# Kernel tuning notes

Hardware: AMD Instinct MI355X
Metric: run time of the kernel (lower is better)

The kernel has to match this reference:

```python
import jax, jax.numpy as jnp
import numpy as np

ALPHA = 3.0   # self.alpha
TAU = 0.1     # contrastive temperature
K = 8         # configs.k (top-k hyperedges per node)


def _scale(x, w, ehy, enod):
    """One scale of incidence_matrix_learn.
    x: [B, L, D] series tokens; w: [ws, D] word tokens;
    ehy: [H, D] hyperedge embedding table; enod: [N, D] node embedding table, N = L + ws.
    Returns (binary incidence matrix [N, H] float32, scalar contrastive loss).
    """
    B = x.shape[0]
    # concat_all[i]: cat(x.permute(0,2,1), word_expanded) -> [B, D, N]
    we = jnp.broadcast_to(w.T[None], (B,) + w.T.shape)          # [B, D, ws]
    concat = jnp.concatenate([jnp.transpose(x, (0, 2, 1)), we], axis=-1)  # [B, D, N]
    N, H = enod.shape[0], ehy.shape[0]
    # adjacency: softmax(relu(alpha * nodeec @ hyperen.T)) along hyperedge dim
    a = enod @ ehy.T                                            # [N, H]
    adj = jax.nn.softmax(jax.nn.relu(ALPHA * a), axis=-1)
    # top-k mask + threshold > 0.5 -> binary incidence matrix
    k = min(H, K)
    _, idx = jax.lax.top_k(adj, k)                              # [N, k]
    mask = jnp.zeros_like(adj).at[jnp.arange(N)[:, None], idx].set(1.0)
    adj_bin = ((adj * mask) > 0.5).astype(jnp.float32)          # [N, H]
    # positives: nodes sharing any hyperedge (build_pos_indices_from_edge_index),
    # equivalent to (A A^T > 0) with self excluded; dropping all-zero columns is a no-op here
    P = (adj_bin @ adj_bin.T > 0) & ~jnp.eye(N, dtype=bool)     # [N, N]
    cnt = P.sum(axis=1)                                         # positives per node
    # acl_loss_batched, vectorized over batch and nodes
    nodes = jnp.transpose(concat, (0, 2, 1))                    # [B, N, D]
    nrm = nodes / jnp.maximum(jnp.linalg.norm(nodes, axis=-1, keepdims=True), 1e-12)
    sim = jnp.einsum('bnd,bmd->bnm', nrm, nrm) / TAU            # [B, N, N]
    denom = jax.nn.logsumexp(sim, axis=-1)                      # [B, N]
    pos_mean = jnp.einsum('bnm,nm->bn', sim, P.astype(sim.dtype)) / jnp.maximum(cnt, 1)
    valid = cnt > 0                                             # [N]
    loss_sum = jnp.sum(jnp.where(valid[None, :], denom - pos_mean, 0.0))
    vc = B * valid.sum()
    loss = jnp.where(vc > 0, loss_sum / jnp.maximum(vc, 1), 0.0)
    return adj_bin, loss


def setup_inputs() -> dict:
    key = jax.random.key(0)
    ks = jax.random.split(key, 8)
    B, D = 64, 512
    return dict(
        x0=jax.random.normal(ks[0], (B, 512, D), dtype=jnp.float32),
        x1=jax.random.normal(ks[1], (B, 256, D), dtype=jnp.float32),
        word0=jax.random.normal(ks[2], (128, D), dtype=jnp.float32),
        word1=jax.random.normal(ks[3], (128, D), dtype=jnp.float32),
        embhy0=jax.random.normal(ks[4], (128, D), dtype=jnp.float32),
        embhy1=jax.random.normal(ks[5], (64, D), dtype=jnp.float32),
        embnod0=jax.random.normal(ks[6], (640, D), dtype=jnp.float32),
        embnod1=jax.random.normal(ks[7], (384, D), dtype=jnp.float32),
    )


def reference(x0, x1, word0, word1, embhy0, embhy1, embnod0, embnod1):
    a0, l0 = _scale(x0, word0, embhy0, embnod0)
    a1, l1 = _scale(x1, word1, embhy1, embnod1)
    return (a0, a1, l0 + l1)
```

## Files before the change

### kernel.cpp

```cpp
#include <hip/hip_runtime.h>


#define DDIM 512
#define BATCH 64
#define NGID 65536

typedef __attribute__((ext_vector_type(8))) short short8;
typedef __attribute__((ext_vector_type(4))) float f32x4;

__constant__ int PAIR_SCALE[21] = {0,0,0,0,0,0,0,0,0,0,0,0,0,0,0, 1,1,1,1,1,1};
__constant__ int PAIR_TU[21]    = {0,0,0,0,0,1,1,1,1,2,2,2,3,3,4, 0,0,0,1,1,2};
__constant__ int PAIR_TV[21]    = {0,1,2,3,4,1,2,3,4,2,3,4,3,4,4, 0,1,2,1,2,2};

__device__ __forceinline__ unsigned short f2bf(float f) {
  unsigned int u = __float_as_uint(f);
  u += 0x7fffu + ((u >> 16) & 1u);
  return (unsigned short)(u >> 16);
}

__device__ __forceinline__ void async16(const void* g, void* l) {
  __builtin_amdgcn_global_load_lds(
      (const __attribute__((address_space(1))) unsigned int*)g,
      (__attribute__((address_space(3))) unsigned int*)l, 16, 0, 0);
}

__global__ __launch_bounds__(256) void prep_kernel(
    const float* __restrict__ enod0, const float* __restrict__ ehy0,
    const float* __restrict__ enod1, const float* __restrict__ ehy1,
    float* __restrict__ adj0, float* __restrict__ adj1,
    int* __restrict__ labels0, int* __restrict__ labels1,
    const float* __restrict__ x0, const float* __restrict__ w0,
    const float* __restrict__ x1, const float* __restrict__ w1,
    unsigned short* __restrict__ nhat0, unsigned short* __restrict__ nhat1,
    float* __restrict__ acc, int* __restrict__ ticket) {
  const int t = threadIdx.x;
  if (blockIdx.x < 1024) {
    if (blockIdx.x == 0 && t == 0) { acc[0] = 0.f; acc[1] = 0.f; ticket[0] = 0; }
    const bool s0 = blockIdx.x < 640;
    const int n = s0 ? blockIdx.x : blockIdx.x - 640;
    const int H = s0 ? 128 : 64;
    const float* enod = s0 ? enod0 : enod1;
    const float* ehy = s0 ? ehy0 : ehy1;
    float* out_adj = s0 ? adj0 : adj1;
    int* labels = s0 ? labels0 : labels1;
    __shared__ float erow[DDIM];
    __shared__ float red[128];
    __shared__ int lab;
    if (t < 128) ((float4*)erow)[t] = ((const float4*)(enod + (size_t)n * DDIM))[t];
    if (t == 0) lab = -1;
    __syncthreads();
    float v = 0.f;
    if (t < H) {
      const float4* hr = (const float4*)(ehy + (size_t)t * DDIM);
      float a = 0.f;
      #pragma unroll 8
      for (int d = 0; d < DDIM / 4; ++d) {
        float4 h = hr[d];
        float4 e = ((const float4*)erow)[d];
        a = fmaf(h.x, e.x, a); a = fmaf(h.y, e.y, a);
        a = fmaf(h.z, e.z, a); a = fmaf(h.w, e.w, a);
      }
      v = fmaxf(0.f, 3.0f * a);
    }
    if (t < 128) red[t] = v;
    __syncthreads();
    for (int s = 64; s > 0; s >>= 1) {
      if (t < s) red[t] = fmaxf(red[t], red[t + s]);
      __syncthreads();
    }
    const float mx = red[0];
    __syncthreads();
    const float e = (t < H) ? __expf(v - mx) : 0.f;
    if (t < 128) red[t] = e;
    __syncthreads();
    for (int s = 64; s > 0; s >>= 1) {
      if (t < s) red[t] += red[t + s];
      __syncthreads();
    }
    const float sum = red[0];
    if (t < H) {
      const float adj = e / sum;
      const float bin = (adj > 0.5f) ? 1.0f : 0.0f;
      out_adj[(size_t)n * H + t] = bin;
      if (bin > 0.f) lab = t;
    }
    __syncthreads();
    if (t == 0) labels[n] = lab;
  } else {
    const int wave = t >> 6;
    const int lane = t & 63;
    const int g = (blockIdx.x - 1024) * 4 + wave;
    const bool s0 = g < BATCH * 640;
    const int gg = s0 ? g : g - BATCH * 640;
    const int N = s0 ? 640 : 384;
    const int L = s0 ? 512 : 256;
    const float* x = s0 ? x0 : x1;
    const float* w = s0 ? w0 : w1;
    unsigned short* nhat = s0 ? nhat0 : nhat1;
    const int b = gg / N;
    const int n = gg - b * N;
    const float* src = (n < L) ? (x + ((size_t)b * L + n) * DDIM)
                               : (w + (size_t)(n - L) * DDIM);
    const float4* rowp = (const float4*)src;
    const float4 v0 = rowp[lane];
    const float4 v1 = rowp[lane + 64];
    float ss = v0.x * v0.x + v0.y * v0.y + v0.z * v0.z + v0.w * v0.w +
               v1.x * v1.x + v1.y * v1.y + v1.z * v1.z + v1.w * v1.w;
    #pragma unroll
    for (int off = 32; off > 0; off >>= 1) ss += __shfl_xor(ss, off);
    const float rinv = 1.0f / fmaxf(sqrtf(ss), 1e-12f);
    ushort4 o0, o1;
    o0.x = f2bf(v0.x * rinv); o0.y = f2bf(v0.y * rinv);
    o0.z = f2bf(v0.z * rinv); o0.w = f2bf(v0.w * rinv);
    o1.x = f2bf(v1.x * rinv); o1.y = f2bf(v1.y * rinv);
    o1.z = f2bf(v1.z * rinv); o1.w = f2bf(v1.w * rinv);
    ushort4* op = (ushort4*)(nhat + ((size_t)b * N + n) * DDIM);
    op[lane] = o0;
    op[lane + 64] = o1;
  }
}

__global__ __launch_bounds__(256) void lse_kernel(
    const unsigned short* __restrict__ nhat0, const int* __restrict__ labels0,
    const unsigned short* __restrict__ nhat1, const int* __restrict__ labels1,
    float2* __restrict__ sp) {
  __shared__ short8 Abuf[3][512];
  __shared__ short8 Bbuf[3][512];
  __shared__ int labU[128], labV[128];
  __shared__ float2 rowBuf[128][2];
  __shared__ float2 colBuf[128][2];

  const int tid = threadIdx.x;
  const int p = blockIdx.x >> 6;
  const int b = blockIdx.x & 63;
  const bool s0 = PAIR_SCALE[p] == 0;
  const int tu = PAIR_TU[p], tv = PAIR_TV[p];
  const bool diag = (tu == tv);
  const int N = s0 ? 640 : 384;
  const unsigned short* nhat = s0 ? nhat0 : nhat1;
  const int* labels = s0 ? labels0 : labels1;
  const int gbase = s0 ? b * 640 : 40960 + b * 384;
  const size_t base = (size_t)b * N * DDIM;

  const int w = tid >> 6, lane = tid & 63;
  const int wr = w >> 1, wc = w & 1;
  const int lrow = lane & 15, lq = lane >> 4;

  if (tid < 128) labU[tid] = labels[tu * 128 + tid];
  else labV[tid - 128] = labels[tv * 128 + (tid - 128)];

  const unsigned short* Asrc = nhat + base + (size_t)tu * 128 * DDIM;
  const unsigned short* Bsrc = nhat + base + (size_t)tv * 128 * DDIM;

  #define STAGE(slot, cc)                                                    \
    do {                                                                     \
      _Pragma("unroll")                                                      \
      for (int i = 0; i < 2; ++i) {                                          \
        const int f = w * 2 + i;                                             \
        const size_t so = (size_t)(f * 16 + lrow) * DDIM + (cc) * 32 + lq * 8;\
        async16(Asrc + so, &Abuf[slot][f * 64]);                             \
        async16(Bsrc + so, &Bbuf[slot][f * 64]);                             \
      }                                                                      \
    } while (0)

  f32x4 acc[4][4];
  #pragma unroll
  for (int mi = 0; mi < 4; ++mi)
    #pragma unroll
    for (int ni = 0; ni < 4; ++ni) acc[mi][ni] = (f32x4){0.f, 0.f, 0.f, 0.f};

  STAGE(0, 0);
  STAGE(1, 1);

  #pragma unroll
  for (int c = 0; c < 16; ++c) {
    if (c < 15) asm volatile("s_waitcnt vmcnt(4)" ::: "memory");
    else        asm volatile("s_waitcnt vmcnt(0)" ::: "memory");
    __builtin_amdgcn_s_barrier();
    if (c < 14) STAGE((c + 2) % 3, c + 2);
    const short8* Ab = &Abuf[c % 3][0];
    const short8* Bb = &Bbuf[c % 3][0];
    short8 am[4], bn[4];
    #pragma unroll
    for (int mi = 0; mi < 4; ++mi) am[mi] = Ab[(wr * 4 + mi) * 64 + lane];
    #pragma unroll
    for (int ni = 0; ni < 4; ++ni) bn[ni] = Bb[(wc * 4 + ni) * 64 + lane];
    #pragma unroll
    for (int mi = 0; mi < 4; ++mi)
      #pragma unroll
      for (int ni = 0; ni < 4; ++ni)
        acc[mi][ni] = __builtin_amdgcn_mfma_f32_16x16x32_bf16(
            am[mi], bn[ni], acc[mi][ni], 0, 0, 0);
  }
  #undef STAGE

  float rSE[4][4], rPOS[4][4];
  float cSE[4] = {0.f, 0.f, 0.f, 0.f};
  float cPOS[4] = {0.f, 0.f, 0.f, 0.f};
  int labn[4][4], labm[4];
  #pragma unroll
  for (int mi = 0; mi < 4; ++mi)
    #pragma unroll
    for (int r = 0; r < 4; ++r) {
      rSE[mi][r] = 0.f; rPOS[mi][r] = 0.f;
      labn[mi][r] = labU[wr * 64 + mi * 16 + lq * 4 + r];
    }
  #pragma unroll
  for (int ni = 0; ni < 4; ++ni) labm[ni] = labV[wc * 64 + ni * 16 + lrow];

  #pragma unroll
  for (int mi = 0; mi < 4; ++mi) {
    const int u_loc = wr * 64 + mi * 16 + lq * 4;
    #pragma unroll
    for (int ni = 0; ni < 4; ++ni) {
      const int v_loc = wc * 64 + ni * 16 + lrow;
      #pragma unroll
      for (int r = 0; r < 4; ++r) {
        const float sim = acc[mi][ni][r] * 10.0f;
        const float e = __expf(sim - 10.0f);
        rSE[mi][r] += e;
        const bool match = (labn[mi][r] >= 0) && (labm[ni] == labn[mi][r]);
        const bool self = diag && (u_loc + r == v_loc);
        if (match && !self) rPOS[mi][r] += sim;
        if (!diag) {
          cSE[ni] += e;
          if (match) cPOS[ni] += sim;
        }
      }
    }
  }

  #pragma unroll
  for (int off = 1; off <= 8; off <<= 1)
    #pragma unroll
    for (int mi = 0; mi < 4; ++mi)
      #pragma unroll
      for (int r = 0; r < 4; ++r) {
        rSE[mi][r] += __shfl_xor(rSE[mi][r], off);
        rPOS[mi][r] += __shfl_xor(rPOS[mi][r], off);
      }
  if (lrow == 0) {
    #pragma unroll
    for (int mi = 0; mi < 4; ++mi)
      #pragma unroll
      for (int r = 0; r < 4; ++r) {
        float2 st; st.x = rSE[mi][r]; st.y = rPOS[mi][r];
        rowBuf[wr * 64 + mi * 16 + lq * 4 + r][wc] = st;
      }
  }
  if (!diag) {
    #pragma unroll
    for (int off = 16; off <= 32; off <<= 1)
      #pragma unroll
      for (int ni = 0; ni < 4; ++ni) {
        cSE[ni] += __shfl_xor(cSE[ni], off);
        cPOS[ni] += __shfl_xor(cPOS[ni], off);
      }
    if (lane < 16) {
      #pragma unroll
      for (int ni = 0; ni < 4; ++ni) {
        float2 st; st.x = cSE[ni]; st.y = cPOS[ni];
        colBuf[wc * 64 + ni * 16 + lrow][wr] = st;
      }
    }
  }
  __syncthreads();
  if (tid < 128) {
    const float2 ra = rowBuf[tid][0], rb = rowBuf[tid][1];
    float2 st; st.x = ra.x + rb.x; st.y = ra.y + rb.y;
    sp[(size_t)tv * NGID + gbase + tu * 128 + tid] = st;
    if (!diag) {
      const float2 ca = colBuf[tid][0], cb = colBuf[tid][1];
      float2 ct; ct.x = ca.x + cb.x; ct.y = ca.y + cb.y;
      sp[(size_t)tu * NGID + gbase + tv * 128 + tid] = ct;
    }
  }
}

__global__ __launch_bounds__(256) void loss_reduce(
    const float2* __restrict__ sp, const int* __restrict__ labels0,
    const int* __restrict__ labels1, float* __restrict__ acc,
    int* __restrict__ ticket, float* __restrict__ lossp) {
  __shared__ int lab0[640], lab1[384];
  __shared__ int hist0[128], hist1[64];
  __shared__ int vcS[2];
  __shared__ float r0[4], r1[4];
  const int t = threadIdx.x;
  if (t < 128) hist0[t] = 0;
  else if (t < 192) hist1[t - 128] = 0;
  if (t < 2) vcS[t] = 0;
  for (int i = t; i < 640; i += 256) lab0[i] = labels0[i];
  for (int i = t; i < 384; i += 256) lab1[i] = labels1[i];
  __syncthreads();
  for (int i = t; i < 640; i += 256)
    if (lab0[i] >= 0) atomicAdd(&hist0[lab0[i]], 1);
  for (int i = t; i < 384; i += 256)
    if (lab1[i] >= 0) atomicAdd(&hist1[lab1[i]], 1);
  __syncthreads();
  int lv0 = 0, lv1 = 0;
  for (int i = t; i < 640; i += 256)
    if (lab0[i] >= 0 && hist0[lab0[i]] >= 2) ++lv0;
  for (int i = t; i < 384; i += 256)
    if (lab1[i] >= 0 && hist1[lab1[i]] >= 2) ++lv1;
  if (lv0 > 0) atomicAdd(&vcS[0], lv0);
  if (lv1 > 0) atomicAdd(&vcS[1], lv1);
  __syncthreads();

  float l0 = 0.f, l1 = 0.f;
  for (int g = blockIdx.x * 256 + t; g < NGID; g += 64 * 256) {
    const bool is0 = g < 40960;
    const int n = is0 ? (g % 640) : ((g - 40960) % 384);
    const int nslots = is0 ? 5 : 3;
    float se = 0.f, pos = 0.f;
    for (int s = 0; s < nslots; ++s) {
      const float2 v = sp[(size_t)s * NGID + g];
      se += v.x; pos += v.y;
    }
    const int lb = is0 ? lab0[n] : lab1[n];
    const int c = (lb >= 0) ? ((is0 ? hist0[lb] : hist1[lb]) - 1) : 0;
    if (c > 0) {
      const float v = (10.0f + logf(se)) - pos / (float)c;
      if (is0) l0 += v; else l1 += v;
    }
  }
  #pragma unroll
  for (int off = 32; off > 0; off >>= 1) {
    l0 += __shfl_xor(l0, off);
    l1 += __shfl_xor(l1, off);
  }
  if ((t & 63) == 0) { r0[t >> 6] = l0; r1[t >> 6] = l1; }
  __syncthreads();
  if (t == 0) {
    atomicAdd(&acc[0], r0[0] + r0[1] + r0[2] + r0[3]);
    atomicAdd(&acc[1], r1[0] + r1[1] + r1[2] + r1[3]);
    __threadfence();
    const int done = atomicAdd(ticket, 1);
    if (done == 63) {
      const float a0v = atomicAdd(&acc[0], 0.0f);
      const float a1v = atomicAdd(&acc[1], 0.0f);
      float l = 0.f;
      if (vcS[0] > 0) l += a0v / (float)(BATCH * vcS[0]);
      if (vcS[1] > 0) l += a1v / (float)(BATCH * vcS[1]);
      lossp[0] = l;
    }
  }
}

extern "C" void kernel_launch(void* const* d_in, const int* in_sizes, int n_in,
                              void* d_out, int out_size, void* d_ws,
                              size_t ws_size, hipStream_t stream) {
  const float* x0 = (const float*)d_in[0];
  const float* x1 = (const float*)d_in[1];
  const float* w0 = (const float*)d_in[2];
  const float* w1 = (const float*)d_in[3];
  const float* ehy0 = (const float*)d_in[4];
  const float* ehy1 = (const float*)d_in[5];
  const float* enod0 = (const float*)d_in[6];
  const float* enod1 = (const float*)d_in[7];

  float* out = (float*)d_out;
  float* adj0 = out;
  float* adj1 = out + 640 * 128;
  float* lossp = out + 640 * 128 + 384 * 64;

  unsigned short* nhat0 = (unsigned short*)d_ws;
  unsigned short* nhat1 = nhat0 + (size_t)BATCH * 640 * DDIM;
  int* ip = (int*)(nhat1 + (size_t)BATCH * 384 * DDIM);
  int* labels0 = ip;
  int* labels1 = labels0 + 640;
  int* ticket = labels1 + 384;
  float* acc = (float*)(ticket + 1);
  float2* sp = (float2*)((((size_t)(acc + 2)) + 255) & ~(size_t)255);

  prep_kernel<<<1024 + 16384, 256, 0, stream>>>(
      enod0, ehy0, enod1, ehy1, adj0, adj1, labels0, labels1,
      x0, w0, x1, w1, nhat0, nhat1, acc, ticket);
  lse_kernel<<<1344, 256, 0, stream>>>(nhat0, labels0, nhat1, labels1, sp);
  loss_reduce<<<64, 256, 0, stream>>>(sp, labels0, labels1, acc, ticket,
                                      lossp);
}
```

Measured before the change: 237.7 us.

## Grid-stride normalize rows and overlay LDS buffers in lse kernel

The normalization part of prep_kernel now runs 1024 blocks, each looping over 16 rows per wave, instead of launching 16384 blocks. This cuts block launch overhead. In lse_kernel, the separate shared arrays become one 48KB buffer that the reduction buffers reuse after a barrier, and labels are loaded straight from global memory into registers. The smaller LDS footprint could allow more resident blocks, but each thread now holds extra registers, and the grid-stride loop does not overlap row loads across iterations.

```diff
diff --git a/kernel.cpp b/kernel.cpp
--- a/kernel.cpp
+++ b/kernel.cpp
@@ -89,34 +89,42 @@
   } else {
     const int wave = t >> 6;
     const int lane = t & 63;
-    const int g = (blockIdx.x - 1024) * 4 + wave;
-    const bool s0 = g < BATCH * 640;
-    const int gg = s0 ? g : g - BATCH * 640;
-    const int N = s0 ? 640 : 384;
-    const int L = s0 ? 512 : 256;
-    const float* x = s0 ? x0 : x1;
-    const float* w = s0 ? w0 : w1;
-    unsigned short* nhat = s0 ? nhat0 : nhat1;
-    const int b = gg / N;
-    const int n = gg - b * N;
-    const float* src = (n < L) ? (x + ((size_t)b * L + n) * DDIM)
-                               : (w + (size_t)(n - L) * DDIM);
-    const float4* rowp = (const float4*)src;
-    const float4 v0 = rowp[lane];
-    const float4 v1 = rowp[lane + 64];
-    float ss = v0.x * v0.x + v0.y * v0.y + v0.z * v0.z + v0.w * v0.w +
-               v1.x * v1.x + v1.y * v1.y + v1.z * v1.z + v1.w * v1.w;
-    #pragma unroll
-    for (int off = 32; off > 0; off >>= 1) ss += __shfl_xor(ss, off);
-    const float rinv = 1.0f / fmaxf(sqrtf(ss), 1e-12f);
-    ushort4 o0, o1;
-    o0.x = f2bf(v0.x * rinv); o0.y = f2bf(v0.y * rinv);
-    o0.z = f2bf(v0.z * rinv); o0.w = f2bf(v0.w * rinv);
-    o1.x = f2bf(v1.x * rinv); o1.y = f2bf(v1.y * rinv);
-    o1.z = f2bf(v1.z * rinv); o1.w = f2bf(v1.w * rinv);
-    ushort4* op = (ushort4*)(nhat + ((size_t)b * N + n) * DDIM);
-    op[lane] = o0;
-    op[lane + 64] = o1;
+    const int wid = (blockIdx.x - 1024) * 4 + wave;
+    for (int it = 0; it < 16; ++it) {
+      const int g = wid + it * 4096;
+      const float* src;
+      unsigned short* dst;
+      if (g < BATCH * 640) {
+        const int b = g / 640;
+        const int n = g - b * 640;
+        src = (n < 512) ? (x0 + ((size_t)b * 512 + n) * DDIM)
+                        : (w0 + (size_t)(n - 512) * DDIM);
+        dst = nhat0 + ((size_t)b * 640 + n) * DDIM;
+      } else {
+        const int gg = g - BATCH * 640;
+        const int b = gg / 384;
+        const int n = gg - b * 384;
+        src = (n < 256) ? (x1 + ((size_t)b * 256 + n) * DDIM)
+                        : (w1 + (size_t)(n - 256) * DDIM);
+        dst = nhat1 + ((size_t)b * 384 + n) * DDIM;
+      }
+      const float4* rowp = (const float4*)src;
+      const float4 v0 = rowp[lane];
+      const float4 v1 = rowp[lane + 64];
+      float ss = v0.x * v0.x + v0.y * v0.y + v0.z * v0.z + v0.w * v0.w +
+                 v1.x * v1.x + v1.y * v1.y + v1.z * v1.z + v1.w * v1.w;
+      #pragma unroll
+      for (int off = 32; off > 0; off >>= 1) ss += __shfl_xor(ss, off);
+      const float rinv = 1.0f / fmaxf(sqrtf(ss), 1e-12f);
+      ushort4 o0, o1;
+      o0.x = f2bf(v0.x * rinv); o0.y = f2bf(v0.y * rinv);
+      o0.z = f2bf(v0.z * rinv); o0.w = f2bf(v0.w * rinv);
+      o1.x = f2bf(v1.x * rinv); o1.y = f2bf(v1.y * rinv);
+      o1.z = f2bf(v1.z * rinv); o1.w = f2bf(v1.w * rinv);
+      ushort4* op = (ushort4*)dst;
+      op[lane] = o0;
+      op[lane + 64] = o1;
+    }
   }
 }
 
@@ -124,11 +132,7 @@
     const unsigned short* __restrict__ nhat0, const int* __restrict__ labels0,
     const unsigned short* __restrict__ nhat1, const int* __restrict__ labels1,
     float2* __restrict__ sp) {
-  __shared__ short8 Abuf[3][512];
-  __shared__ short8 Bbuf[3][512];
-  __shared__ int labU[128], labV[128];
-  __shared__ float2 rowBuf[128][2];
-  __shared__ float2 colBuf[128][2];
+  __shared__ char smem[49152];
 
   const int tid = threadIdx.x;
   const int p = blockIdx.x >> 6;
@@ -146,20 +150,30 @@
   const int wr = w >> 1, wc = w & 1;
   const int lrow = lane & 15, lq = lane >> 4;
 
-  if (tid < 128) labU[tid] = labels[tu * 128 + tid];
-  else labV[tid - 128] = labels[tv * 128 + (tid - 128)];
+  int labn[4][4], labm[4];
+  #pragma unroll
+  for (int mi = 0; mi < 4; ++mi)
+    #pragma unroll
+    for (int r = 0; r < 4; ++r)
+      labn[mi][r] = labels[tu * 128 + wr * 64 + mi * 16 + lq * 4 + r];
+  #pragma unroll
+  for (int ni = 0; ni < 4; ++ni)
+    labm[ni] = labels[tv * 128 + wc * 64 + ni * 16 + lrow];
+  asm volatile("s_waitcnt vmcnt(0)" ::: "memory");
 
   const unsigned short* Asrc = nhat + base + (size_t)tu * 128 * DDIM;
   const unsigned short* Bsrc = nhat + base + (size_t)tv * 128 * DDIM;
 
+  #define SLOTA(s) ((short8*)(smem + (s) * 16384))
+  #define SLOTB(s) ((short8*)(smem + (s) * 16384 + 8192))
   #define STAGE(slot, cc)                                                    \
     do {                                                                     \
       _Pragma("unroll")                                                      \
       for (int i = 0; i < 2; ++i) {                                          \
         const int f = w * 2 + i;                                             \
         const size_t so = (size_t)(f * 16 + lrow) * DDIM + (cc) * 32 + lq * 8;\
-        async16(Asrc + so, &Abuf[slot][f * 64]);                             \
-        async16(Bsrc + so, &Bbuf[slot][f * 64]);                             \
+        async16(Asrc + so, SLOTA(slot) + f * 64);                            \
+        async16(Bsrc + so, SLOTB(slot) + f * 64);                            \
       }                                                                      \
     } while (0)
 
@@ -178,8 +192,8 @@
     else        asm volatile("s_waitcnt vmcnt(0)" ::: "memory");
     __builtin_amdgcn_s_barrier();
     if (c < 14) STAGE((c + 2) % 3, c + 2);
-    const short8* Ab = &Abuf[c % 3][0];
-    const short8* Bb = &Bbuf[c % 3][0];
+    const short8* Ab = SLOTA(c % 3);
+    const short8* Bb = SLOTB(c % 3);
     short8 am[4], bn[4];
     #pragma unroll
     for (int mi = 0; mi < 4; ++mi) am[mi] = Ab[(wr * 4 + mi) * 64 + lane];
@@ -194,19 +208,17 @@
   }
   #undef STAGE
 
+  __syncthreads();
+  float2 (*rowBuf)[2] = (float2(*)[2])smem;
+  float2 (*colBuf)[2] = (float2(*)[2])(smem + 2048);
+
   float rSE[4][4], rPOS[4][4];
   float cSE[4] = {0.f, 0.f, 0.f, 0.f};
   float cPOS[4] = {0.f, 0.f, 0.f, 0.f};
-  int labn[4][4], labm[4];
   #pragma unroll
   for (int mi = 0; mi < 4; ++mi)
     #pragma unroll
-    for (int r = 0; r < 4; ++r) {
-      rSE[mi][r] = 0.f; rPOS[mi][r] = 0.f;
-      labn[mi][r] = labU[wr * 64 + mi * 16 + lq * 4 + r];
-    }
-  #pragma unroll
-  for (int ni = 0; ni < 4; ++ni) labm[ni] = labV[wc * 64 + ni * 16 + lrow];
+    for (int r = 0; r < 4; ++r) { rSE[mi][r] = 0.f; rPOS[mi][r] = 0.f; }
 
   #pragma unroll
   for (int mi = 0; mi < 4; ++mi) {
@@ -372,7 +384,7 @@
   float* acc = (float*)(ticket + 1);
   float2* sp = (float2*)((((size_t)(acc + 2)) + 255) & ~(size_t)255);
 
-  prep_kernel<<<1024 + 16384, 256, 0, stream>>>(
+  prep_kernel<<<2048, 256, 0, stream>>>(
       enod0, ehy0, enod1, ehy1, adj0, adj1, labels0, labels1,
       x0, w0, x1, w1, nhat0, nhat1, acc, ticket);
   lse_kernel<<<1344, 256, 0, stream>>>(nhat0, labels0, nhat1, labels1, sp);
```

New measurement: 234.5 us. Within noise of the previous version (-1.3%).
